# Kernel tuning notes

Hardware: AMD Instinct MI355X
Metric: run time of the kernel (lower is better)

The kernel has to match this reference:

```python
import jax, jax.numpy as jnp
import numpy as np


def conv1x1(x, w, b):
    # 1x1 Conv2d: x [B,C,H,W], w [O,C], b [O] -> [B,O,H,W]
    return jnp.einsum('bchw,oc->bohw', x, w) + b[None, :, None, None]


def setup_inputs() -> dict:
    key = jax.random.key(0)
    ks = jax.random.split(key, 10)
    B, C, Ci, H, W = 4, 64, 32, 64, 64
    s = 0.05
    return {
        'supp_feature': jax.random.normal(ks[0], (B, C, H, W), jnp.float32),
        'ref_feature': jax.random.normal(ks[1], (B, C, H, W), jnp.float32),
        'theta_w': jax.random.normal(ks[2], (Ci, C), jnp.float32) * s,
        'theta_b': jax.random.normal(ks[3], (Ci,), jnp.float32) * s,
        'phi_w': jax.random.normal(ks[4], (Ci, C), jnp.float32) * s,
        'phi_b': jax.random.normal(ks[5], (Ci,), jnp.float32) * s,
        'g_w': jax.random.normal(ks[6], (Ci, C), jnp.float32) * s,
        'g_b': jax.random.normal(ks[7], (Ci,), jnp.float32) * s,
        'w_w': jax.random.normal(ks[8], (C, Ci), jnp.float32) * s,
        'w_b': jax.random.normal(ks[9], (C,), jnp.float32) * s,
    }


def reference(supp_feature, ref_feature, theta_w, theta_b, phi_w, phi_b,
              g_w, g_b, w_w, w_b):
    B, C, H, W = supp_feature.shape
    Ci = theta_w.shape[0]
    N = H * W
    theta_x = conv1x1(supp_feature, theta_w, theta_b).reshape(B, Ci, N)  # [B,Ci,N]
    phi_y = conv1x1(ref_feature, phi_w, phi_b).reshape(B, Ci, N)        # [B,Ci,M]
    g_y = conv1x1(ref_feature, g_w, g_b).reshape(B, Ci, N)              # [B,Ci,M]
    # f[b,n,m] = <theta_x[b,:,n], phi_y[b,:,m]>  (unscaled)
    f = jnp.einsum('bcn,bcm->bnm', theta_x, phi_y)
    # NOTE: softmax over dim=1 (the QUERY axis n), matching F.softmax(f, dim=1)
    f_div_C = jax.nn.softmax(f, axis=1)
    # x1[b,c,n] = sum_m f_div_C[b,n,m] * g_y[b,c,m]
    x1 = jnp.einsum('bnm,bcm->bcn', f_div_C, g_y).reshape(B, Ci, H, W)
    z = supp_feature + conv1x1(x1, w_w, w_b)
    return z
```

## Files before the change

kernel.cpp:

```cpp
#include <hip/hip_runtime.h>

#define C_ 64
#define CI_ 32
#define N_ 4096
#define LOG2E 1.4426950408889634f

typedef __attribute__((ext_vector_type(8))) short bf16x8;
typedef __attribute__((ext_vector_type(4))) float f32x4;

__device__ __forceinline__ unsigned short f2bf_rne(float f) {
  unsigned u = __builtin_bit_cast(unsigned, f);
  unsigned r = (u + 0x7FFFu + ((u >> 16) & 1u)) >> 16;
  return (unsigned short)r;
}
__device__ __forceinline__ unsigned pack_bf2(float lo, float hi) {
  unsigned a = (__builtin_bit_cast(unsigned, lo) + 0x8000u) >> 16;
  unsigned b = (__builtin_bit_cast(unsigned, hi) + 0x8000u) & 0xFFFF0000u;
  return a | b;
}
__device__ __forceinline__ float bf2f(unsigned short v) {
  return __builtin_bit_cast(float, (unsigned)v << 16);
}
__device__ __forceinline__ void dma16(const void* gp, const void* lp) {
  __builtin_amdgcn_global_load_lds(
      (const __attribute__((address_space(1))) unsigned*)(unsigned long long)gp,
      (__attribute__((address_space(3))) unsigned*)(unsigned)(unsigned long long)lp,
      16, 0, 0);
}


__global__ __launch_bounds__(256) void k1_proj(
    const float* __restrict__ supp, const float* __restrict__ ref,
    const float* __restrict__ tw, const float* __restrict__ tb,
    const float* __restrict__ pw, const float* __restrict__ pb,
    const float* __restrict__ gw, const float* __restrict__ gb,
    unsigned short* __restrict__ theta, unsigned short* __restrict__ phi2,
    unsigned short* __restrict__ g2)
{
  const int proj = blockIdx.x >> 8;
  const int rr = blockIdx.x & 255;
  const int b = rr >> 6;
  const int n0 = (rr & 63) << 6;
  const int o = __builtin_amdgcn_readfirstlane(threadIdx.x >> 6);
  const int lane = threadIdx.x & 63;
  const int n = n0 + lane;

  __shared__ float gL[CI_][66];

  const float *W, *bias, *src;
  if (proj == 0)      { W = tw; bias = tb; src = supp; }
  else if (proj == 1) { W = pw; bias = pb; src = ref; }
  else                { W = gw; bias = gb; src = ref; }

  const float* x = src + (size_t)b * (C_ * N_) + n;
  const float* Wo = W + o * 8 * C_;
  float acc[8];
#pragma unroll
  for (int k = 0; k < 8; k++) acc[k] = bias[o * 8 + k];
#pragma unroll 8
  for (int c = 0; c < C_; c++) {
    float v = x[(size_t)c * N_];
#pragma unroll
    for (int k = 0; k < 8; k++) acc[k] = fmaf(Wo[k * C_ + c], v, acc[k]);
  }

  if (proj == 0) {
    unsigned pk[4];
#pragma unroll
    for (int k = 0; k < 4; k++)
      pk[k] = (unsigned)f2bf_rne(acc[2 * k] * LOG2E) |
              ((unsigned)f2bf_rne(acc[2 * k + 1] * LOG2E) << 16);
    *(uint4*)(theta + (((size_t)b * N_ + n) << 5) + o * 8) = *(uint4*)pk;
  } else if (proj == 1) {
    unsigned pk[4];
#pragma unroll
    for (int k = 0; k < 4; k++)
      pk[k] = (unsigned)f2bf_rne(acc[2 * k]) |
              ((unsigned)f2bf_rne(acc[2 * k + 1]) << 16);
    size_t off = (((size_t)b * 128 + (n >> 5)) << 10) + o * 256 + (n & 31) * 8;
    *(uint4*)(phi2 + off) = *(uint4*)pk;
  } else {
#pragma unroll
    for (int k = 0; k < 8; k++) gL[o * 8 + k][lane] = acc[k];
    __syncthreads();
    const int t = threadIdx.x;
    const int c = t >> 7;
    const int rr2 = t & 127;
    const int q = rr2 >> 5;
    const int i = rr2 & 31;
    const float* g0 = &gL[i][c * 32 + 4 * q];
    unsigned pk[4];
    pk[0] = pack_bf2(g0[0], g0[1]);
    pk[1] = pack_bf2(g0[2], g0[3]);
    pk[2] = pack_bf2(g0[16], g0[17]);
    pk[3] = pack_bf2(g0[18], g0[19]);
    size_t off = (((size_t)b * 128 + (n0 >> 5) + c) << 10) + rr2 * 8;
    *(uint4*)(g2 + off) = *(uint4*)pk;
  }
}

__global__ __launch_bounds__(1024) void k2_den(
    const unsigned short* __restrict__ theta, const unsigned short* __restrict__ phi2,
    float* __restrict__ rden)
{
  const int tid = threadIdx.x;
  const int wave = tid >> 6;
  const int lane = tid & 63;
  const int b = blockIdx.x >> 6;
  const int mbase = (blockIdx.x & 63) << 6;
  const int row16 = lane & 15;
  const int quad = lane >> 4;

  bf16x8 bf[4];
#pragma unroll
  for (int f = 0; f < 4; f++) {
    int ch = (mbase >> 5) + (f >> 1);
    int r = ((f & 1) << 4) + row16;
    bf[f] = *(const bf16x8*)(phi2 +
        (((size_t)b * 128 + ch) << 10) + (quad << 8) + r * 8);
  }

  const unsigned short* abase = theta +
      (((size_t)b * N_ + wave * 256 + row16) << 5) + (quad << 3);

  f32x4 zero = {0.f, 0.f, 0.f, 0.f};
  float dd[16];
#pragma unroll
  for (int k = 0; k < 16; k++) dd[k] = 0.f;

  bf16x8 a0 = *(const bf16x8*)abase;
  bf16x8 a1 = *(const bf16x8*)(abase + 512);
#pragma unroll 2
  for (int it = 0; it < 16; it++) {
    int itn = it + 2 <= 15 ? it + 2 : 15;
    bf16x8 an = *(const bf16x8*)(abase + ((size_t)itn << 9));
#pragma unroll
    for (int f = 0; f < 4; f++) {
      f32x4 ff = __builtin_amdgcn_mfma_f32_16x16x32_bf16(a0, bf[f], zero, 0, 0, 0);
#pragma unroll
      for (int r = 0; r < 4; r++) dd[f * 4 + r] += __builtin_amdgcn_exp2f(ff[r]);
    }
    a0 = a1; a1 = an;
  }

  __shared__ float denp[16][64];
#pragma unroll
  for (int f = 0; f < 4; f++) {
    float v = (dd[f * 4] + dd[f * 4 + 1]) + (dd[f * 4 + 2] + dd[f * 4 + 3]);
    v += __shfl_xor(v, 16);
    v += __shfl_xor(v, 32);
    if (lane < 16) denp[wave][f * 16 + lane] = v;
  }
  __syncthreads();

  if (tid < 64) {
    int p = tid;
    int q = (p >> 3) & 3, j = p & 7;
    int ml = (p & 32) + 4 * q + (j & 3) + ((j >> 2) << 4);
    float den = 0.f;
#pragma unroll
    for (int w = 0; w < 16; w++) den += denp[w][ml];
    rden[(((size_t)b * 128 + (mbase >> 5) + (p >> 5)) << 5) + (p & 31)] = 1.0f / den;
  }
}

__global__ __launch_bounds__(256, 4) void k3_attn(
    const unsigned short* __restrict__ theta, const unsigned short* __restrict__ phi2,
    const unsigned short* __restrict__ g2, const float* __restrict__ rden,
    unsigned short* __restrict__ x1p)
{
  const int tid = threadIdx.x;
  const int w = tid >> 6;
  const int lane = tid & 63;
  const int b = blockIdx.x >> 8;
  const int nt = (blockIdx.x >> 3) & 31;
  const int ms = blockIdx.x & 7;
  const int row16 = lane & 15;
  const int quad = lane >> 4;

  __shared__ __align__(16) unsigned short SB[4 * 2048];

  const int nbase = nt * 128 + w * 32;
  bf16x8 tB0 = *(const bf16x8*)(theta + (((size_t)b * N_ + nbase + row16) << 5) + (quad << 3));
  bf16x8 tB1 = *(const bf16x8*)(theta + (((size_t)b * N_ + nbase + 16 + row16) << 5) + (quad << 3));

  const size_t chunkb = (size_t)b * 128 + ms * 16;

  f32x4 zero = {0.f, 0.f, 0.f, 0.f};
  f32x4 xa0 = zero, xb0 = zero, xa1 = zero, xb1 = zero;

  for (int ph = 0; ph < 4; ph++) {
#pragma unroll
    for (int s = 0; s < 4; s++) {
      int idx = w * 4 + s;
      int c = idx >> 2;
      int seg = idx & 3;
      const unsigned short* src = (seg >= 2 ? g2 : phi2) +
          ((chunkb + ph * 4 + c) << 10) + ((seg & 1) << 9) + lane * 8;
      const unsigned short* dst = SB + c * 2048 + (seg >= 2 ? 1024 : 0) + ((seg & 1) << 9);
      dma16(src, dst);
    }
    __syncthreads();
#pragma unroll
    for (int c = 0; c < 4; c++) {
      const unsigned short* lphi = SB + c * 2048;
      const unsigned short* lg = SB + c * 2048 + 1024;
      bf16x8 pA0 = *(const bf16x8*)(lphi + (quad << 8) + row16 * 8);
      bf16x8 pA1 = *(const bf16x8*)(lphi + (quad << 8) + (row16 + 16) * 8);
      bf16x8 gA0 = *(const bf16x8*)(lg + (quad << 8) + row16 * 8);
      bf16x8 gA1 = *(const bf16x8*)(lg + (quad << 8) + (row16 + 16) * 8);
      const float* rp = rden + ((chunkb + ph * 4 + c) << 5) + (quad << 3);
      f32x4 r0 = *(const f32x4*)rp;
      f32x4 r1 = *(const f32x4*)(rp + 4);

      f32x4 f00 = __builtin_amdgcn_mfma_f32_16x16x32_bf16(pA0, tB0, zero, 0, 0, 0);
      f32x4 f10 = __builtin_amdgcn_mfma_f32_16x16x32_bf16(pA1, tB0, zero, 0, 0, 0);
      f32x4 f01 = __builtin_amdgcn_mfma_f32_16x16x32_bf16(pA0, tB1, zero, 0, 0, 0);
      f32x4 f11 = __builtin_amdgcn_mfma_f32_16x16x32_bf16(pA1, tB1, zero, 0, 0, 0);

      uint4 d0, d1;
      d0.x = pack_bf2(__builtin_amdgcn_exp2f(f00[0]) * r0[0],
                      __builtin_amdgcn_exp2f(f00[1]) * r0[1]);
      d0.y = pack_bf2(__builtin_amdgcn_exp2f(f00[2]) * r0[2],
                      __builtin_amdgcn_exp2f(f00[3]) * r0[3]);
      d0.z = pack_bf2(__builtin_amdgcn_exp2f(f10[0]) * r1[0],
                      __builtin_amdgcn_exp2f(f10[1]) * r1[1]);
      d0.w = pack_bf2(__builtin_amdgcn_exp2f(f10[2]) * r1[2],
                      __builtin_amdgcn_exp2f(f10[3]) * r1[3]);
      d1.x = pack_bf2(__builtin_amdgcn_exp2f(f01[0]) * r0[0],
                      __builtin_amdgcn_exp2f(f01[1]) * r0[1]);
      d1.y = pack_bf2(__builtin_amdgcn_exp2f(f01[2]) * r0[2],
                      __builtin_amdgcn_exp2f(f01[3]) * r0[3]);
      d1.z = pack_bf2(__builtin_amdgcn_exp2f(f11[0]) * r1[0],
                      __builtin_amdgcn_exp2f(f11[1]) * r1[1]);
      d1.w = pack_bf2(__builtin_amdgcn_exp2f(f11[2]) * r1[2],
                      __builtin_amdgcn_exp2f(f11[3]) * r1[3]);
      bf16x8 Pb0 = __builtin_bit_cast(bf16x8, d0);
      bf16x8 Pb1 = __builtin_bit_cast(bf16x8, d1);

      xa0 = __builtin_amdgcn_mfma_f32_16x16x32_bf16(gA0, Pb0, xa0, 0, 0, 0);
      xb0 = __builtin_amdgcn_mfma_f32_16x16x32_bf16(gA1, Pb0, xb0, 0, 0, 0);
      xa1 = __builtin_amdgcn_mfma_f32_16x16x32_bf16(gA0, Pb1, xa1, 0, 0, 0);
      xb1 = __builtin_amdgcn_mfma_f32_16x16x32_bf16(gA1, Pb1, xb1, 0, 0, 0);
    }
    __syncthreads();
  }

  size_t obase = ((size_t)(b * 8 + ms) * CI_) * N_;
#pragma unroll
  for (int r = 0; r < 4; r++) {
    size_t i0 = (size_t)(quad * 4 + r) * N_;
    size_t i1 = (size_t)(16 + quad * 4 + r) * N_;
    x1p[obase + i0 + nbase + row16] = f2bf_rne(xa0[r]);
    x1p[obase + i0 + nbase + 16 + row16] = f2bf_rne(xa1[r]);
    x1p[obase + i1 + nbase + row16] = f2bf_rne(xb0[r]);
    x1p[obase + i1 + nbase + 16 + row16] = f2bf_rne(xb1[r]);
  }
}

__global__ __launch_bounds__(256) void k4_out(
    const unsigned short* __restrict__ x1p, const float* __restrict__ supp,
    const float* __restrict__ ww, const float* __restrict__ wb,
    float* __restrict__ out)
{
  const int tid = threadIdx.x;
  const int b = blockIdx.x >> 7;
  const int n0 = (blockIdx.x & 127) << 5;

  __shared__ float x1L[CI_ * 33];
  __shared__ float wwL[C_ * 33];

  for (int e = tid; e < C_ * CI_; e += 256)
    wwL[(e >> 5) * 33 + (e & 31)] = ww[e];
  for (int e = tid; e < CI_ * 32; e += 256) {
    int i = e >> 5, nl = e & 31;
    size_t a = ((size_t)b * 8 * CI_ + i) * N_ + n0 + nl;
    float s = 0.f;
#pragma unroll
    for (int q = 0; q < 8; q++) s += bf2f(x1p[a + (size_t)q * CI_ * N_]);
    x1L[i * 33 + nl] = s;
  }
  __syncthreads();

  const int c = tid >> 2;
  const int nl0 = (tid & 3) << 3;
  float a[8];
  float bv = wb[c];
#pragma unroll
  for (int j = 0; j < 8; j++) a[j] = bv;
#pragma unroll 8
  for (int i = 0; i < CI_; i++) {
    float wv = wwL[c * 33 + i];
    const float* xr = &x1L[i * 33 + nl0];
#pragma unroll
    for (int j = 0; j < 8; j++) a[j] = fmaf(wv, xr[j], a[j]);
  }
  size_t ob = ((size_t)b * C_ + c) * N_ + n0 + nl0;
  float4 s0 = *(const float4*)(supp + ob);
  float4 s1 = *(const float4*)(supp + ob + 4);
  float4 o0, o1;
  o0.x = a[0] + s0.x; o0.y = a[1] + s0.y; o0.z = a[2] + s0.z; o0.w = a[3] + s0.w;
  o1.x = a[4] + s1.x; o1.y = a[5] + s1.y; o1.z = a[6] + s1.z; o1.w = a[7] + s1.w;
  *(float4*)(out + ob) = o0;
  *(float4*)(out + ob + 4) = o1;
}

extern "C" void kernel_launch(void* const* d_in, const int* in_sizes, int n_in,
                              void* d_out, int out_size, void* d_ws, size_t ws_size,
                              hipStream_t stream)
{
  const float* supp = (const float*)d_in[0];
  const float* ref  = (const float*)d_in[1];
  const float* tw   = (const float*)d_in[2];
  const float* tb   = (const float*)d_in[3];
  const float* pw   = (const float*)d_in[4];
  const float* pb   = (const float*)d_in[5];
  const float* gw   = (const float*)d_in[6];
  const float* gb   = (const float*)d_in[7];
  const float* ww   = (const float*)d_in[8];
  const float* wb   = (const float*)d_in[9];
  float* out = (float*)d_out;

  char* ws = (char*)d_ws;
  unsigned short* theta = (unsigned short*)ws;
  unsigned short* phi2  = (unsigned short*)(ws + (1u << 20));
  unsigned short* g2    = (unsigned short*)(ws + (2u << 20));
  float*          rden  = (float*)(ws + (3u << 20));
  unsigned short* x1p   = (unsigned short*)(ws + (4u << 20));

  hipLaunchKernelGGL(k1_proj, dim3(768), dim3(256), 0, stream,
                     supp, ref, tw, tb, pw, pb, gw, gb, theta, phi2, g2);
  hipLaunchKernelGGL(k2_den, dim3(256), dim3(1024), 0, stream,
                     theta, phi2, rden);
  hipLaunchKernelGGL(k3_attn, dim3(1024), dim3(256), 0, stream,
                     theta, phi2, g2, rden, x1p);
  hipLaunchKernelGGL(k4_out, dim3(512), dim3(256), 0, stream,
                     x1p, supp, ww, wb, out);
}
```

Baseline: 119.1 us.

## Fuse output projection into attention kernel with in-block split-M reduction

Merges the attention and output-projection kernels. Each 1024-thread block now handles 64 query positions across all keys, with four wave groups splitting the key range and double-buffered LDS staging, then reduces the partial sums in shared memory. The final 1x1 conv is done with MFMA against a bf16 permuted weight, which the denominator kernel prepares. This removes the x1 partial buffer's global round trip and one kernel launch. The cost is fewer blocks (256), a barrier on every key chunk, and uncoalesced scalar output stores.

```diff
diff --git a/kernel.cpp b/kernel.cpp
--- a/kernel.cpp
+++ b/kernel.cpp
@@ -17,9 +17,6 @@
   unsigned a = (__builtin_bit_cast(unsigned, lo) + 0x8000u) >> 16;
   unsigned b = (__builtin_bit_cast(unsigned, hi) + 0x8000u) & 0xFFFF0000u;
   return a | b;
-}
-__device__ __forceinline__ float bf2f(unsigned short v) {
-  return __builtin_bit_cast(float, (unsigned)v << 16);
 }
 __device__ __forceinline__ void dma16(const void* gp, const void* lp) {
   __builtin_amdgcn_global_load_lds(
@@ -101,7 +98,8 @@
 
 __global__ __launch_bounds__(1024) void k2_den(
     const unsigned short* __restrict__ theta, const unsigned short* __restrict__ phi2,
-    float* __restrict__ rden)
+    const float* __restrict__ ww, float* __restrict__ rden,
+    unsigned short* __restrict__ ww2)
 {
   const int tid = threadIdx.x;
   const int wave = tid >> 6;
@@ -111,6 +109,14 @@
   const int row16 = lane & 15;
   const int quad = lane >> 4;
 
+  if (blockIdx.x == 0) {
+    for (int e = tid; e < C_ * CI_; e += 1024) {
+      int p = e & 31;
+      int i = 4 * ((p >> 3) & 3) + (p & 3) + 16 * ((p >> 2) & 1);
+      ww2[e] = f2bf_rne(ww[(e >> 5) * CI_ + i]);
+    }
+  }
+
   bf16x8 bf[4];
 #pragma unroll
   for (int f = 0; f < 4; f++) {
@@ -164,145 +170,109 @@
   }
 }
 
-__global__ __launch_bounds__(256, 4) void k3_attn(
+__global__ __launch_bounds__(1024) void k3_attn(
     const unsigned short* __restrict__ theta, const unsigned short* __restrict__ phi2,
     const unsigned short* __restrict__ g2, const float* __restrict__ rden,
-    unsigned short* __restrict__ x1p)
+    const unsigned short* __restrict__ ww2, const float* __restrict__ wb,
+    const float* __restrict__ supp, float* __restrict__ out)
 {
   const int tid = threadIdx.x;
   const int w = tid >> 6;
   const int lane = tid & 63;
-  const int b = blockIdx.x >> 8;
-  const int nt = (blockIdx.x >> 3) & 31;
-  const int ms = blockIdx.x & 7;
+  const int b = blockIdx.x >> 6;
+  const int n0 = (blockIdx.x & 63) << 6;
+  const int ns = w & 3;
+  const int q = w >> 2;
   const int row16 = lane & 15;
   const int quad = lane >> 4;
 
-  __shared__ __align__(16) unsigned short SB[4 * 2048];
-
-  const int nbase = nt * 128 + w * 32;
-  bf16x8 tB0 = *(const bf16x8*)(theta + (((size_t)b * N_ + nbase + row16) << 5) + (quad << 3));
-  bf16x8 tB1 = *(const bf16x8*)(theta + (((size_t)b * N_ + nbase + 16 + row16) << 5) + (quad << 3));
-
-  const size_t chunkb = (size_t)b * 128 + ms * 16;
+  __shared__ __align__(16) unsigned short SB[2][4][2048];
+
+  bf16x8 tB = *(const bf16x8*)(theta +
+      (((size_t)b * N_ + n0 + ns * 16 + row16) << 5) + (quad << 3));
+
+  const size_t chb = (size_t)b * 128;
+  const int sq = w >> 2;
+  const int sp = w & 3;
 
   f32x4 zero = {0.f, 0.f, 0.f, 0.f};
-  f32x4 xa0 = zero, xb0 = zero, xa1 = zero, xb1 = zero;
-
-  for (int ph = 0; ph < 4; ph++) {
-#pragma unroll
-    for (int s = 0; s < 4; s++) {
-      int idx = w * 4 + s;
-      int c = idx >> 2;
-      int seg = idx & 3;
-      const unsigned short* src = (seg >= 2 ? g2 : phi2) +
-          ((chunkb + ph * 4 + c) << 10) + ((seg & 1) << 9) + lane * 8;
-      const unsigned short* dst = SB + c * 2048 + (seg >= 2 ? 1024 : 0) + ((seg & 1) << 9);
-      dma16(src, dst);
-    }
+  f32x4 xa = zero, xb = zero;
+
+  {
+    const unsigned short* src = (sp >= 2 ? g2 : phi2) +
+        ((chb + sq * 32) << 10) + ((size_t)(sp & 1) << 9) + lane * 8;
+    dma16(src, &SB[0][sq][(sp >= 2 ? 1024 : 0) + ((sp & 1) << 9)]);
+  }
+  __syncthreads();
+
+  for (int ph = 0; ph < 32; ph++) {
+    const int buf = ph & 1;
+    if (ph + 1 < 32) {
+      const unsigned short* src = (sp >= 2 ? g2 : phi2) +
+          ((chb + sq * 32 + ph + 1) << 10) + ((size_t)(sp & 1) << 9) + lane * 8;
+      dma16(src, &SB[buf ^ 1][sq][(sp >= 2 ? 1024 : 0) + ((sp & 1) << 9)]);
+    }
+    const unsigned short* base = &SB[buf][q][0];
+    bf16x8 pA0 = *(const bf16x8*)(base + (quad << 8) + row16 * 8);
+    bf16x8 pA1 = *(const bf16x8*)(base + (quad << 8) + (row16 + 16) * 8);
+    bf16x8 gA0 = *(const bf16x8*)(base + 1024 + (quad << 8) + row16 * 8);
+    bf16x8 gA1 = *(const bf16x8*)(base + 1024 + (quad << 8) + (row16 + 16) * 8);
+    const float* rp = rden + ((chb + q * 32 + ph) << 5) + (quad << 3);
+    f32x4 r0 = *(const f32x4*)rp;
+    f32x4 r1 = *(const f32x4*)(rp + 4);
+
+    f32x4 f0 = __builtin_amdgcn_mfma_f32_16x16x32_bf16(pA0, tB, zero, 0, 0, 0);
+    f32x4 f1 = __builtin_amdgcn_mfma_f32_16x16x32_bf16(pA1, tB, zero, 0, 0, 0);
+
+    uint4 d;
+    d.x = pack_bf2(__builtin_amdgcn_exp2f(f0[0]) * r0[0],
+                   __builtin_amdgcn_exp2f(f0[1]) * r0[1]);
+    d.y = pack_bf2(__builtin_amdgcn_exp2f(f0[2]) * r0[2],
+                   __builtin_amdgcn_exp2f(f0[3]) * r0[3]);
+    d.z = pack_bf2(__builtin_amdgcn_exp2f(f1[0]) * r1[0],
+                   __builtin_amdgcn_exp2f(f1[1]) * r1[1]);
+    d.w = pack_bf2(__builtin_amdgcn_exp2f(f1[2]) * r1[2],
+                   __builtin_amdgcn_exp2f(f1[3]) * r1[3]);
+    bf16x8 Pb = __builtin_bit_cast(bf16x8, d);
+
+    xa = __builtin_amdgcn_mfma_f32_16x16x32_bf16(gA0, Pb, xa, 0, 0, 0);
+    xb = __builtin_amdgcn_mfma_f32_16x16x32_bf16(gA1, Pb, xb, 0, 0, 0);
     __syncthreads();
-#pragma unroll
-    for (int c = 0; c < 4; c++) {
-      const unsigned short* lphi = SB + c * 2048;
-      const unsigned short* lg = SB + c * 2048 + 1024;
-      bf16x8 pA0 = *(const bf16x8*)(lphi + (quad << 8) + row16 * 8);
-      bf16x8 pA1 = *(const bf16x8*)(lphi + (quad << 8) + (row16 + 16) * 8);
-      bf16x8 gA0 = *(const bf16x8*)(lg + (quad << 8) + row16 * 8);
-      bf16x8 gA1 = *(const bf16x8*)(lg + (quad << 8) + (row16 + 16) * 8);
-      const float* rp = rden + ((chunkb + ph * 4 + c) << 5) + (quad << 3);
-      f32x4 r0 = *(const f32x4*)rp;
-      f32x4 r1 = *(const f32x4*)(rp + 4);
-
-      f32x4 f00 = __builtin_amdgcn_mfma_f32_16x16x32_bf16(pA0, tB0, zero, 0, 0, 0);
-      f32x4 f10 = __builtin_amdgcn_mfma_f32_16x16x32_bf16(pA1, tB0, zero, 0, 0, 0);
-      f32x4 f01 = __builtin_amdgcn_mfma_f32_16x16x32_bf16(pA0, tB1, zero, 0, 0, 0);
-      f32x4 f11 = __builtin_amdgcn_mfma_f32_16x16x32_bf16(pA1, tB1, zero, 0, 0, 0);
-
-      uint4 d0, d1;
-      d0.x = pack_bf2(__builtin_amdgcn_exp2f(f00[0]) * r0[0],
-                      __builtin_amdgcn_exp2f(f00[1]) * r0[1]);
-      d0.y = pack_bf2(__builtin_amdgcn_exp2f(f00[2]) * r0[2],
-                      __builtin_amdgcn_exp2f(f00[3]) * r0[3]);
-      d0.z = pack_bf2(__builtin_amdgcn_exp2f(f10[0]) * r1[0],
-                      __builtin_amdgcn_exp2f(f10[1]) * r1[1]);
-      d0.w = pack_bf2(__builtin_amdgcn_exp2f(f10[2]) * r1[2],
-                      __builtin_amdgcn_exp2f(f10[3]) * r1[3]);
-      d1.x = pack_bf2(__builtin_amdgcn_exp2f(f01[0]) * r0[0],
-                      __builtin_amdgcn_exp2f(f01[1]) * r0[1]);
-      d1.y = pack_bf2(__builtin_amdgcn_exp2f(f01[2]) * r0[2],
-                      __builtin_amdgcn_exp2f(f01[3]) * r0[3]);
-      d1.z = pack_bf2(__builtin_amdgcn_exp2f(f11[0]) * r1[0],
-                      __builtin_amdgcn_exp2f(f11[1]) * r1[1]);
-      d1.w = pack_bf2(__builtin_amdgcn_exp2f(f11[2]) * r1[2],
-                      __builtin_amdgcn_exp2f(f11[3]) * r1[3]);
-      bf16x8 Pb0 = __builtin_bit_cast(bf16x8, d0);
-      bf16x8 Pb1 = __builtin_bit_cast(bf16x8, d1);
-
-      xa0 = __builtin_amdgcn_mfma_f32_16x16x32_bf16(gA0, Pb0, xa0, 0, 0, 0);
-      xb0 = __builtin_amdgcn_mfma_f32_16x16x32_bf16(gA1, Pb0, xb0, 0, 0, 0);
-      xa1 = __builtin_amdgcn_mfma_f32_16x16x32_bf16(gA0, Pb1, xa1, 0, 0, 0);
-      xb1 = __builtin_amdgcn_mfma_f32_16x16x32_bf16(gA1, Pb1, xb1, 0, 0, 0);
-    }
-    __syncthreads();
-  }
-
-  size_t obase = ((size_t)(b * 8 + ms) * CI_) * N_;
-#pragma unroll
-  for (int r = 0; r < 4; r++) {
-    size_t i0 = (size_t)(quad * 4 + r) * N_;
-    size_t i1 = (size_t)(16 + quad * 4 + r) * N_;
-    x1p[obase + i0 + nbase + row16] = f2bf_rne(xa0[r]);
-    x1p[obase + i0 + nbase + 16 + row16] = f2bf_rne(xa1[r]);
-    x1p[obase + i1 + nbase + row16] = f2bf_rne(xb0[r]);
-    x1p[obase + i1 + nbase + 16 + row16] = f2bf_rne(xb1[r]);
-  }
-}
-
-__global__ __launch_bounds__(256) void k4_out(
-    const unsigned short* __restrict__ x1p, const float* __restrict__ supp,
-    const float* __restrict__ ww, const float* __restrict__ wb,
-    float* __restrict__ out)
-{
-  const int tid = threadIdx.x;
-  const int b = blockIdx.x >> 7;
-  const int n0 = (blockIdx.x & 127) << 5;
-
-  __shared__ float x1L[CI_ * 33];
-  __shared__ float wwL[C_ * 33];
-
-  for (int e = tid; e < C_ * CI_; e += 256)
-    wwL[(e >> 5) * 33 + (e & 31)] = ww[e];
-  for (int e = tid; e < CI_ * 32; e += 256) {
-    int i = e >> 5, nl = e & 31;
-    size_t a = ((size_t)b * 8 * CI_ + i) * N_ + n0 + nl;
-    float s = 0.f;
-#pragma unroll
-    for (int q = 0; q < 8; q++) s += bf2f(x1p[a + (size_t)q * CI_ * N_]);
-    x1L[i * 33 + nl] = s;
+  }
+
+  float* part = (float*)SB;
+  if (q) {
+    float* dst = part + ((((q - 1) * 4 + ns) * 64 + lane) << 3);
+#pragma unroll
+    for (int r = 0; r < 4; r++) { dst[r] = xa[r]; dst[4 + r] = xb[r]; }
   }
   __syncthreads();
-
-  const int c = tid >> 2;
-  const int nl0 = (tid & 3) << 3;
-  float a[8];
-  float bv = wb[c];
-#pragma unroll
-  for (int j = 0; j < 8; j++) a[j] = bv;
-#pragma unroll 8
-  for (int i = 0; i < CI_; i++) {
-    float wv = wwL[c * 33 + i];
-    const float* xr = &x1L[i * 33 + nl0];
-#pragma unroll
-    for (int j = 0; j < 8; j++) a[j] = fmaf(wv, xr[j], a[j]);
-  }
-  size_t ob = ((size_t)b * C_ + c) * N_ + n0 + nl0;
-  float4 s0 = *(const float4*)(supp + ob);
-  float4 s1 = *(const float4*)(supp + ob + 4);
-  float4 o0, o1;
-  o0.x = a[0] + s0.x; o0.y = a[1] + s0.y; o0.z = a[2] + s0.z; o0.w = a[3] + s0.w;
-  o1.x = a[4] + s1.x; o1.y = a[5] + s1.y; o1.z = a[6] + s1.z; o1.w = a[7] + s1.w;
-  *(float4*)(out + ob) = o0;
-  *(float4*)(out + ob + 4) = o1;
+  if (q == 0) {
+#pragma unroll
+    for (int e = 0; e < 3; e++) {
+      const float* s = part + (((e * 4 + ns) * 64 + lane) << 3);
+#pragma unroll
+      for (int r = 0; r < 4; r++) { xa[r] += s[r]; xb[r] += s[4 + r]; }
+    }
+    uint4 d;
+    d.x = pack_bf2(xa[0], xa[1]);
+    d.y = pack_bf2(xa[2], xa[3]);
+    d.z = pack_bf2(xb[0], xb[1]);
+    d.w = pack_bf2(xb[2], xb[3]);
+    bf16x8 Bx = __builtin_bit_cast(bf16x8, d);
+    const int nloc = n0 + ns * 16 + row16;
+#pragma unroll
+    for (int ct = 0; ct < 4; ct++) {
+      bf16x8 aw = *(const bf16x8*)(ww2 + (ct * 16 + row16) * CI_ + (quad << 3));
+      f32x4 o = __builtin_amdgcn_mfma_f32_16x16x32_bf16(aw, Bx, zero, 0, 0, 0);
+#pragma unroll
+      for (int r = 0; r < 4; r++) {
+        int c = ct * 16 + quad * 4 + r;
+        size_t ob = ((size_t)b * C_ + c) * N_ + nloc;
+        out[ob] = o[r] + wb[c] + supp[ob];
+      }
+    }
+  }
 }
 
 extern "C" void kernel_launch(void* const* d_in, const int* in_sizes, int n_in,
@@ -326,14 +296,12 @@
   unsigned short* phi2  = (unsigned short*)(ws + (1u << 20));
   unsigned short* g2    = (unsigned short*)(ws + (2u << 20));
   float*          rden  = (float*)(ws + (3u << 20));
-  unsigned short* x1p   = (unsigned short*)(ws + (4u << 20));
+  unsigned short* ww2   = (unsigned short*)(ws + (3u << 20) + 65536);
 
   hipLaunchKernelGGL(k1_proj, dim3(768), dim3(256), 0, stream,
                      supp, ref, tw, tb, pw, pb, gw, gb, theta, phi2, g2);
   hipLaunchKernelGGL(k2_den, dim3(256), dim3(1024), 0, stream,
-                     theta, phi2, rden);
-  hipLaunchKernelGGL(k3_attn, dim3(1024), dim3(256), 0, stream,
-                     theta, phi2, g2, rden, x1p);
-  hipLaunchKernelGGL(k4_out, dim3(512), dim3(256), 0, stream,
-                     x1p, supp, ww, wb, out);
-}
+                     theta, phi2, ww, rden, ww2);
+  hipLaunchKernelGGL(k3_attn, dim3(256), dim3(1024), 0, stream,
+                     theta, phi2, g2, rden, ww2, wb, supp, out);
+}
```

New measurement: 117.3 us. Within noise of the previous version (-1.5%).
